# Performance work log

Measured on AMD Instinct MI355X. Metric: run time of the kernel, lower is better.

Reference implementation:

```python
import jax, jax.numpy as jnp
import numpy as np

N_NODES = 100_000
N_EDGES = 1_600_000
F_IN = 32
F_OUT = 32
DIM = 2
K = 5                      # kernel_size per dim (open spline)
KTOT = K ** DIM            # 25 kernel weight matrices
S = 2 ** DIM               # 4 nonzero linear-B-spline basis terms per edge
NEG_SLOPE = 0.2

# offsets over the 2^DIM corners of the spline cell, [S, DIM]
_OFFSETS = np.array([[(s >> d) & 1 for d in range(DIM)] for s in range(S)], dtype=np.int32)
_STRIDES = np.array([K ** d for d in range(DIM)], dtype=np.int32)


def _spline_basis(pseudo):
    """Degree-1 open B-spline basis. pseudo: [E, DIM] in [0,1].
    Returns basis [E, S] and kernel-weight indices widx [E, S]."""
    offsets = jnp.asarray(_OFFSETS)
    strides = jnp.asarray(_STRIDES)
    p = pseudo * (K - 1)                         # open spline scaling
    fl = jnp.floor(p)
    frac = p - fl                                # [E, DIM]
    b = jnp.where(offsets[None] == 0, 1.0 - frac[:, None, :], frac[:, None, :])
    basis = jnp.prod(b, axis=-1)                 # [E, S]
    idx = jnp.clip(fl.astype(jnp.int32)[:, None, :] + offsets[None], 0, K - 1)
    widx = jnp.sum(idx * strides, axis=-1)       # [E, S] in [0, KTOT)
    return basis, widx


def setup_inputs() -> dict:
    key = jax.random.key(0)
    ks = jax.random.split(key, 7)
    x = jax.random.normal(ks[0], (N_NODES, F_IN), dtype=jnp.float32)
    edge_index = jax.random.randint(ks[1], (2, N_EDGES), 0, N_NODES)
    pseudo = jax.random.uniform(ks[2], (N_EDGES, DIM), dtype=jnp.float32)
    bound = 1.0 / np.sqrt(KTOT * F_IN)           # matches reset_parameters uniform(size, ...)
    weight = jax.random.uniform(ks[3], (KTOT, F_IN, F_OUT), jnp.float32, -bound, bound)
    root_weight = jax.random.uniform(ks[4], (F_IN, F_OUT), jnp.float32, -bound, bound)
    att_weight = jax.random.uniform(ks[5], (2 * F_OUT,), jnp.float32, -bound, bound)
    bias = jax.random.uniform(ks[6], (F_OUT,), jnp.float32, -bound, bound)
    return {"x": x, "edge_index": edge_index, "pseudo": pseudo, "weight": weight,
            "root_weight": root_weight, "att_weight": att_weight, "bias": bias}


def reference(x, edge_index, pseudo, weight, root_weight, att_weight, bias):
    row, col = edge_index[0], edge_index[1]      # row = target, col = source
    basis, widx = _spline_basis(pseudo)          # [E,S], [E,S]

    # Precompute x @ W_k for every kernel weight: [N, KTOT, F_OUT]
    xw = jnp.einsum('nf,kfo->nko', x, weight)
    flat = col[:, None] * KTOT + widx            # [E, S] flat (node, kernel) index
    gathered = xw.reshape(-1, F_OUT)[flat]       # [E, S, F_OUT]
    msg = jnp.einsum('es,esf->ef', basis, gathered)  # spline-weighted edge messages

    x_root = x @ root_weight                     # [N, F_OUT]

    # GAT-style attention logits: cat([x_root[row], msg]) . att_weight
    alpha = x_root[row] @ att_weight[:F_OUT] + msg @ att_weight[F_OUT:]
    alpha = jnp.where(alpha > 0, alpha, NEG_SLOPE * alpha)  # leaky relu

    # segment softmax over incoming edges of each target node
    amax = jax.ops.segment_max(alpha, row, num_segments=N_NODES)
    amax = jnp.where(jnp.isfinite(amax), amax, 0.0)
    ex = jnp.exp(alpha - amax[row])
    denom = jax.ops.segment_sum(ex, row, num_segments=N_NODES)
    att = ex / (denom[row] + 1e-16)

    out = jax.ops.segment_sum(msg * att[:, None], row, num_segments=N_NODES)
    return out + x_root + bias
```

## Files before the change

### kernel.cpp

```cpp
#include <hip/hip_runtime.h>
#include <stdint.h>

#define N_NODES 100000
#define N_EDGES 1600000
#define NBLK_SCAN 391

typedef __attribute__((ext_vector_type(8))) short short8;
typedef __attribute__((ext_vector_type(4))) float float4v;

__device__ __forceinline__ unsigned short f32_to_bf16(float f) {
  uint32_t u = __float_as_uint(f);
  u += 0x7fffu + ((u >> 16) & 1u);
  return (unsigned short)(u >> 16);
}
__device__ __forceinline__ float bf16_to_f32(unsigned short h) {
  return __uint_as_float(((uint32_t)h) << 16);
}

__global__ __launch_bounds__(256) void k_zero(
    const float* __restrict__ weight, const float* __restrict__ root_w,
    int* __restrict__ deg, unsigned short* __restrict__ wbf) {
  int tid = threadIdx.x;
  int b = blockIdx.x;
  int i = b * 256 + tid;
  if (i < N_NODES) deg[i] = 0;
  if (b < 100) {
    int e = i;
    int km = e >> 10;
    int rem = e & 1023;
    int kk = rem >> 5;
    int fo = rem & 31;
    int t = km * 2 + (fo >> 4);
    int c = fo & 15;
    int q = kk >> 3, j = kk & 7;
    wbf[((t * 4 + q) * 16 + c) * 8 + j] = f32_to_bf16(weight[e]);
  } else if (b == 100) {
    for (int idx = tid; idx < 1024; idx += 256) {
      int kk = idx >> 5;
      int fo = idx & 31;
      int t = 50 + (fo >> 4);
      int c = fo & 15;
      int q = kk >> 3, j = kk & 7;
      wbf[((t * 4 + q) * 16 + c) * 8 + j] = f32_to_bf16(root_w[idx]);
    }
  }
}

__global__ __launch_bounds__(256) void k1_xw(
    const float* __restrict__ x, const unsigned short* __restrict__ wbf,
    const int* __restrict__ ei, const float* __restrict__ att_w,
    const float* __restrict__ bias,
    int* __restrict__ deg, unsigned short* __restrict__ rank,
    unsigned short* __restrict__ xw, float* __restrict__ out,
    float* __restrict__ r_dot) {
  __shared__ __align__(16) unsigned short ot[16 * 808];
  __shared__ float xr[16][33];
  int tid = threadIdx.x;
  int b = blockIdx.x;

  int e = b * 256 + tid;
  int rk = atomicAdd(&deg[ei[e]], 1);

  int wave = tid >> 6, lane = tid & 63;
  int quad = lane >> 4, c16 = lane & 15;
  int n0 = b * 16;
  const float* xp = x + (size_t)(n0 + c16) * 32 + quad * 8;
  float4 a0 = *reinterpret_cast<const float4*>(xp);
  float4 a1 = *reinterpret_cast<const float4*>(xp + 4);
  short8 af;
  af[0] = (short)f32_to_bf16(a0.x); af[1] = (short)f32_to_bf16(a0.y);
  af[2] = (short)f32_to_bf16(a0.z); af[3] = (short)f32_to_bf16(a0.w);
  af[4] = (short)f32_to_bf16(a1.x); af[5] = (short)f32_to_bf16(a1.y);
  af[6] = (short)f32_to_bf16(a1.z); af[7] = (short)f32_to_bf16(a1.w);

  for (int t = wave; t < 52; t += 4) {
    short8 bf = *reinterpret_cast<const short8*>(wbf + ((t * 4 + quad) * 16 + c16) * 8);
    float4v acc = {0.f, 0.f, 0.f, 0.f};
    acc = __builtin_amdgcn_mfma_f32_16x16x32_bf16(af, bf, acc, 0, 0, 0);
    if (t < 50) {
      int cg = t * 16 + c16;
#pragma unroll
      for (int r = 0; r < 4; r++) ot[(quad * 4 + r) * 808 + cg] = f32_to_bf16(acc[r]);
    } else {
      int f = (t - 50) * 16 + c16;
#pragma unroll
      for (int r = 0; r < 4; r++) xr[quad * 4 + r][f] = acc[r];
    }
  }
  __syncthreads();

  const uint4* src = (const uint4*)ot;
  uint4* dst = (uint4*)(xw + (size_t)n0 * 800);
  for (int i = tid; i < 1600; i += 256) {
    int r = i / 100;
    int c = i - r * 100;
    dst[r * 100 + c] = src[r * 101 + c];
  }
  for (int idx = tid; idx < 512; idx += 256) {
    int n = idx >> 5, f = idx & 31;
    out[(n0 + n) * 32 + f] = xr[n][f] + bias[f];
  }
  if (tid < 16) {
    float s = 0.f;
#pragma unroll
    for (int f = 0; f < 32; f++) s += xr[tid][f] * att_w[f];
    r_dot[n0 + tid] = s;
  }
  rank[e] = (unsigned short)rk;
}

__global__ __launch_bounds__(256) void kscan1(const int* __restrict__ deg,
                                              int* __restrict__ incl,
                                              int* __restrict__ bsum) {
  __shared__ int s[256];
  int tid = threadIdx.x;
  int i = blockIdx.x * 256 + tid;
  int v = (i < N_NODES) ? deg[i] : 0;
  s[tid] = v;
  __syncthreads();
  for (int d = 1; d < 256; d <<= 1) {
    int t = (tid >= d) ? s[tid - d] : 0;
    __syncthreads();
    s[tid] += t;
    __syncthreads();
  }
  if (i < N_NODES) incl[i] = s[tid];
  if (tid == 255) bsum[blockIdx.x] = s[255];
}

__global__ __launch_bounds__(512) void kscan2(const int* __restrict__ bsum,
                                              int* __restrict__ bbase) {
  __shared__ int s[512];
  int tid = threadIdx.x;
  int v = (tid < NBLK_SCAN) ? bsum[tid] : 0;
  s[tid] = v;
  __syncthreads();
  for (int d = 1; d < 512; d <<= 1) {
    int t = (tid >= d) ? s[tid - d] : 0;
    __syncthreads();
    s[tid] += t;
    __syncthreads();
  }
  if (tid < NBLK_SCAN) bbase[tid] = s[tid] - v;
}

__global__ __launch_bounds__(256) void kscan3(const int* __restrict__ deg,
                                              int* __restrict__ offs,
                                              const int* __restrict__ bbase) {
  int i = blockIdx.x * 256 + threadIdx.x;
  if (i < N_NODES) offs[i] = offs[i] - deg[i] + bbase[i >> 8];
  if (i == 0) offs[N_NODES] = N_EDGES;
}

__global__ __launch_bounds__(256) void kscatter(
    const int* __restrict__ ei, const float* __restrict__ pseudo,
    const int* __restrict__ offs, const unsigned short* __restrict__ rank,
    uint2* __restrict__ epack) {
  int tid = threadIdx.x;
  int base = blockIdx.x * 2048;
#pragma unroll
  for (int k = 0; k < 8; k++) {
    int e = base + k * 256 + tid;
    if (e < N_EDGES) {
      int r = ei[e];
      int c = ei[N_EDGES + e];
      int pos = offs[r] + (int)rank[e];
      float p0 = pseudo[2 * e] * 4.f;
      float p1 = pseudo[2 * e + 1] * 4.f;
      float fl0 = floorf(p0), fl1 = floorf(p1);
      float fr0 = p0 - fl0, fr1 = p1 - fl1;
      int i0 = (int)fl0, i1 = (int)fl1;
      int a0 = min(i0, 4), a0p = min(i0 + 1, 4);
      int a1 = 5 * min(i1, 4), a1p = 5 * min(i1 + 1, 4);
      unsigned long long w0 = (unsigned long long)(a0 + a1);
      unsigned long long w1 = (unsigned long long)(a0p + a1);
      unsigned long long w2 = (unsigned long long)(a0 + a1p);
      unsigned long long w3 = (unsigned long long)(a0p + a1p);
      unsigned long long q0 = (unsigned long long)__float2uint_rn(fr0 * 8191.f);
      unsigned long long q1 = (unsigned long long)__float2uint_rn(fr1 * 8191.f);
      unsigned long long v = (unsigned long long)(unsigned int)c |
                             (w0 << 17) | (w1 << 22) | (w2 << 27) | (w3 << 32) |
                             (q0 << 37) | (q1 << 50);
      uint2 pk;
      pk.x = (unsigned int)v;
      pk.y = (unsigned int)(v >> 32);
      epack[pos] = pk;
    }
  }
}

__device__ __forceinline__ void decode_pk(uint2 pk, int& col, int& w0, int& w1,
                                          int& w2, int& w3, float& fr0, float& fr1) {
  unsigned long long v = ((unsigned long long)pk.y << 32) | pk.x;
  col = (int)(v & 0x1FFFF);
  w0 = (int)((v >> 17) & 31); w1 = (int)((v >> 22) & 31);
  w2 = (int)((v >> 27) & 31); w3 = (int)((v >> 32) & 31);
  fr0 = (float)(unsigned int)((v >> 37) & 8191) * (1.f / 8191.f);
  fr1 = (float)(unsigned int)((v >> 50) & 8191) * (1.f / 8191.f);
}

__device__ __forceinline__ void edge_step(uint2 pk, const unsigned short* __restrict__ xwf,
                                          float a2, float rd, float& acc, float& den) {
  int col, w0, w1, w2, w3; float fr0, fr1;
  decode_pk(pk, col, w0, w1, w2, w3, fr0, fr1);
  const unsigned short* base = xwf + (size_t)col * 800;
  float g0 = bf16_to_f32(base[w0 * 32]);
  float g1 = bf16_to_f32(base[w1 * 32]);
  float g2 = bf16_to_f32(base[w2 * 32]);
  float g3 = bf16_to_f32(base[w3 * 32]);
  float c0 = 1.f - fr0, c1 = 1.f - fr1;
  float msg = c1 * (c0 * g0 + fr0 * g1) + fr1 * (c0 * g2 + fr0 * g3);
  float t = msg * a2;
#pragma unroll
  for (int m = 16; m >= 1; m >>= 1) t += __shfl_xor(t, m);
  float alpha = rd + t;
  alpha = alpha > 0.f ? alpha : 0.2f * alpha;
  float ex = __expf(alpha);
  acc += msg * ex;
  den += ex;
}

__global__ __launch_bounds__(256) void k2_csr(
    const int* __restrict__ offs, const uint2* __restrict__ epack,
    const unsigned short* __restrict__ xw, const float* __restrict__ r_dot,
    const float* __restrict__ att_w, float* __restrict__ out) {
  int tid = threadIdx.x;
  int wave = tid >> 6, lane = tid & 63;
  int node = blockIdx.x * 4 + wave;
  if (node >= N_NODES) return;
  int f = lane & 31, half = lane >> 5;
  float a2 = att_w[32 + f];
  float rd = r_dot[node];
  int s0 = offs[node], s1 = offs[node + 1];
  const unsigned short* xwf = xw + f;
  float acc = 0.f, den = 0.f;
  int i = s0 + half;

  for (; i + 6 < s1; i += 8) {
    uint2 p[4];
    p[0] = epack[i];     p[1] = epack[i + 2];
    p[2] = epack[i + 4]; p[3] = epack[i + 6];
    int col[4], w0[4], w1[4], w2[4], w3[4];
    float fr0[4], fr1[4];
#pragma unroll
    for (int u = 0; u < 4; u++)
      decode_pk(p[u], col[u], w0[u], w1[u], w2[u], w3[u], fr0[u], fr1[u]);
    float g0[4], g1[4], g2[4], g3[4];
#pragma unroll
    for (int u = 0; u < 4; u++) {
      const unsigned short* base = xwf + (size_t)col[u] * 800;
      g0[u] = bf16_to_f32(base[w0[u] * 32]);
      g1[u] = bf16_to_f32(base[w1[u] * 32]);
      g2[u] = bf16_to_f32(base[w2[u] * 32]);
      g3[u] = bf16_to_f32(base[w3[u] * 32]);
    }
    float msg[4], t[4];
#pragma unroll
    for (int u = 0; u < 4; u++) {
      float c0 = 1.f - fr0[u], c1 = 1.f - fr1[u];
      msg[u] = c1 * (c0 * g0[u] + fr0[u] * g1[u]) + fr1[u] * (c0 * g2[u] + fr0[u] * g3[u]);
      t[u] = msg[u] * a2;
    }
#pragma unroll
    for (int m = 16; m >= 1; m >>= 1) {
      t[0] += __shfl_xor(t[0], m);
      t[1] += __shfl_xor(t[1], m);
      t[2] += __shfl_xor(t[2], m);
      t[3] += __shfl_xor(t[3], m);
    }
#pragma unroll
    for (int u = 0; u < 4; u++) {
      float alpha = rd + t[u];
      alpha = alpha > 0.f ? alpha : 0.2f * alpha;
      float ex = __expf(alpha);
      acc += msg[u] * ex;
      den += ex;
    }
  }
  for (; i < s1; i += 2) edge_step(epack[i], xwf, a2, rd, acc, den);

  acc += __shfl_xor(acc, 32);
  den += __shfl_xor(den, 32);
  if (half == 0) out[node * 32 + f] += acc / (den + 1e-16f);
}

extern "C" void kernel_launch(void* const* d_in, const int* in_sizes, int n_in,
                              void* d_out, int out_size, void* d_ws, size_t ws_size,
                              hipStream_t stream) {
  const float* x      = (const float*)d_in[0];
  const int*   ei     = (const int*)d_in[1];
  const float* pseudo = (const float*)d_in[2];
  const float* weight = (const float*)d_in[3];
  const float* root_w = (const float*)d_in[4];
  const float* att_w  = (const float*)d_in[5];
  const float* bias   = (const float*)d_in[6];
  float* out = (float*)d_out;

  char* ws = (char*)d_ws;
  unsigned short* xw   = (unsigned short*)ws;
  float* r_dot         = (float*)(ws + 160000000);
  unsigned short* wbf  = (unsigned short*)(ws + 160400000);
  int* deg             = (int*)(ws + 160453504);
  int* offs            = (int*)(ws + 160853504);
  int* bsum            = (int*)(ws + 161253520);
  int* bbase           = (int*)(ws + 161255120);
  unsigned short* rank = (unsigned short*)(ws + 161256720);
  uint2* epack         = (uint2*)(ws + 164456720);

  hipLaunchKernelGGL(k_zero, dim3(NBLK_SCAN), dim3(256), 0, stream,
                     weight, root_w, deg, wbf);
  hipLaunchKernelGGL(k1_xw, dim3(6250), dim3(256), 0, stream,
                     x, wbf, ei, att_w, bias, deg, rank, xw, out, r_dot);
  hipLaunchKernelGGL(kscan1, dim3(NBLK_SCAN), dim3(256), 0, stream, deg, offs, bsum);
  hipLaunchKernelGGL(kscan2, dim3(1), dim3(512), 0, stream, bsum, bbase);
  hipLaunchKernelGGL(kscan3, dim3(NBLK_SCAN), dim3(256), 0, stream, deg, offs, bbase);
  hipLaunchKernelGGL(kscatter, dim3(782), dim3(256), 0, stream,
                     ei, pseudo, offs, rank, epack);
  hipLaunchKernelGGL(k2_csr, dim3(25000), dim3(256), 0, stream,
                     offs, epack, xw, r_dot, att_w, out);
}
```

Before: 336.8 us.

## Precompute per-node attention dots and move softmax exp into scatter; single-pass scan

Projects each node's 25 xw rows onto the attention vector in k1 (ydot). The scatter kernel then computes each edge's attention logit and exp from four bilinear-interpolated scalars and packs the bf16 exp into the edge record. This removes the per-edge 32-lane shuffle reduction and exp from the CSR aggregation kernel. The three-kernel scan is also replaced by a single decoupled-lookback scan, which cuts two launches. The costs are coarser quantisation (8-bit fractions, bf16 exp and ydot), extra ydot storage and gathers, and a spin-wait lookback that relies on tiles being scheduled in order.

```diff
diff --git a/kernel.cpp b/kernel.cpp
--- a/kernel.cpp
+++ b/kernel.cpp
@@ -19,11 +19,14 @@
 
 __global__ __launch_bounds__(256) void k_zero(
     const float* __restrict__ weight, const float* __restrict__ root_w,
-    int* __restrict__ deg, unsigned short* __restrict__ wbf) {
+    int* __restrict__ deg, unsigned short* __restrict__ wbf,
+    unsigned long long* __restrict__ tilepack, int* __restrict__ tilectr) {
   int tid = threadIdx.x;
   int b = blockIdx.x;
   int i = b * 256 + tid;
   if (i < N_NODES) deg[i] = 0;
+  if (i < NBLK_SCAN) tilepack[i] = 0ull;
+  if (i == 0) *tilectr = 0;
   if (b < 100) {
     int e = i;
     int km = e >> 10;
@@ -52,14 +55,17 @@
     const float* __restrict__ bias,
     int* __restrict__ deg, unsigned short* __restrict__ rank,
     unsigned short* __restrict__ xw, float* __restrict__ out,
-    float* __restrict__ r_dot) {
+    float* __restrict__ r_dot, unsigned short* __restrict__ ydot) {
   __shared__ __align__(16) unsigned short ot[16 * 808];
   __shared__ float xr[16][33];
+  __shared__ float a2s[32];
   int tid = threadIdx.x;
   int b = blockIdx.x;
 
   int e = b * 256 + tid;
   int rk = atomicAdd(&deg[ei[e]], 1);
+
+  if (tid < 32) a2s[tid] = att_w[32 + tid];
 
   int wave = tid >> 6, lane = tid & 63;
   int quad = lane >> 4, c16 = lane & 15;
@@ -96,6 +102,14 @@
     int c = i - r * 100;
     dst[r * 100 + c] = src[r * 101 + c];
   }
+  for (int idx = tid; idx < 400; idx += 256) {
+    int n = idx & 15;
+    int k = idx >> 4;
+    float s = 0.f;
+#pragma unroll
+    for (int ff = 0; ff < 32; ff++) s += bf16_to_f32(ot[n * 808 + k * 32 + ff]) * a2s[ff];
+    ydot[(size_t)(n0 + n) * 25 + k] = f32_to_bf16(s);
+  }
   for (int idx = tid; idx < 512; idx += 256) {
     int n = idx >> 5, f = idx & 31;
     out[(n0 + n) * 32 + f] = xr[n][f] + bias[f];
@@ -109,12 +123,16 @@
   rank[e] = (unsigned short)rk;
 }
 
-__global__ __launch_bounds__(256) void kscan1(const int* __restrict__ deg,
-                                              int* __restrict__ incl,
-                                              int* __restrict__ bsum) {
+__global__ __launch_bounds__(256) void k_scan(
+    const int* __restrict__ deg, int* __restrict__ offs,
+    int* __restrict__ tilectr, unsigned long long* __restrict__ tilepack) {
   __shared__ int s[256];
+  __shared__ int sh_tile, sh_excl;
   int tid = threadIdx.x;
-  int i = blockIdx.x * 256 + tid;
+  if (tid == 0) sh_tile = atomicAdd(tilectr, 1);
+  __syncthreads();
+  int tile = sh_tile;
+  int i = tile * 256 + tid;
   int v = (i < N_NODES) ? deg[i] : 0;
   s[tid] = v;
   __syncthreads();
@@ -124,160 +142,127 @@
     s[tid] += t;
     __syncthreads();
   }
-  if (i < N_NODES) incl[i] = s[tid];
-  if (tid == 255) bsum[blockIdx.x] = s[255];
-}
-
-__global__ __launch_bounds__(512) void kscan2(const int* __restrict__ bsum,
-                                              int* __restrict__ bbase) {
-  __shared__ int s[512];
-  int tid = threadIdx.x;
-  int v = (tid < NBLK_SCAN) ? bsum[tid] : 0;
-  s[tid] = v;
+  int incl = s[tid];
+  int agg = s[255];
+  if (tid == 0) {
+    unsigned long long init = ((tile == 0) ? (2ull << 32) : (1ull << 32)) | (unsigned int)agg;
+    __hip_atomic_store(&tilepack[tile], init, __ATOMIC_RELEASE, __HIP_MEMORY_SCOPE_AGENT);
+    if (tile == 0) sh_excl = 0;
+  }
+  if (tile > 0 && tid < 64) {
+    int excl = 0;
+    int base = tile - 1;
+    while (true) {
+      int look = base - tid;
+      unsigned long long pk;
+      if (look >= 0) {
+        do {
+          pk = __hip_atomic_load(&tilepack[look], __ATOMIC_ACQUIRE, __HIP_MEMORY_SCOPE_AGENT);
+        } while ((pk >> 32) == 0);
+      } else {
+        pk = (2ull << 32);
+      }
+      unsigned long long m2 = __ballot((pk >> 32) == 2);
+      int lim = (m2 == 0ull) ? 64 : (__ffsll(m2) - 1);
+      int val = (tid <= lim) ? (int)(unsigned int)pk : 0;
+#pragma unroll
+      for (int m = 1; m < 64; m <<= 1) val += __shfl_xor(val, m);
+      excl += val;
+      if (lim < 64) break;
+      base -= 64;
+    }
+    if (tid == 0) {
+      __hip_atomic_store(&tilepack[tile], (2ull << 32) | (unsigned int)(excl + agg),
+                         __ATOMIC_RELEASE, __HIP_MEMORY_SCOPE_AGENT);
+      sh_excl = excl;
+    }
+  }
   __syncthreads();
-  for (int d = 1; d < 512; d <<= 1) {
-    int t = (tid >= d) ? s[tid - d] : 0;
-    __syncthreads();
-    s[tid] += t;
-    __syncthreads();
-  }
-  if (tid < NBLK_SCAN) bbase[tid] = s[tid] - v;
-}
-
-__global__ __launch_bounds__(256) void kscan3(const int* __restrict__ deg,
-                                              int* __restrict__ offs,
-                                              const int* __restrict__ bbase) {
-  int i = blockIdx.x * 256 + threadIdx.x;
-  if (i < N_NODES) offs[i] = offs[i] - deg[i] + bbase[i >> 8];
-  if (i == 0) offs[N_NODES] = N_EDGES;
+  if (i < N_NODES) offs[i] = sh_excl + incl - v;
+  if (i == N_NODES - 1) offs[N_NODES] = N_EDGES;
 }
 
 __global__ __launch_bounds__(256) void kscatter(
     const int* __restrict__ ei, const float* __restrict__ pseudo,
     const int* __restrict__ offs, const unsigned short* __restrict__ rank,
+    const float* __restrict__ r_dot, const unsigned short* __restrict__ ydot,
     uint2* __restrict__ epack) {
-  int tid = threadIdx.x;
-  int base = blockIdx.x * 2048;
-#pragma unroll
-  for (int k = 0; k < 8; k++) {
-    int e = base + k * 256 + tid;
-    if (e < N_EDGES) {
-      int r = ei[e];
-      int c = ei[N_EDGES + e];
-      int pos = offs[r] + (int)rank[e];
-      float p0 = pseudo[2 * e] * 4.f;
-      float p1 = pseudo[2 * e + 1] * 4.f;
-      float fl0 = floorf(p0), fl1 = floorf(p1);
-      float fr0 = p0 - fl0, fr1 = p1 - fl1;
-      int i0 = (int)fl0, i1 = (int)fl1;
-      int a0 = min(i0, 4), a0p = min(i0 + 1, 4);
-      int a1 = 5 * min(i1, 4), a1p = 5 * min(i1 + 1, 4);
-      unsigned long long w0 = (unsigned long long)(a0 + a1);
-      unsigned long long w1 = (unsigned long long)(a0p + a1);
-      unsigned long long w2 = (unsigned long long)(a0 + a1p);
-      unsigned long long w3 = (unsigned long long)(a0p + a1p);
-      unsigned long long q0 = (unsigned long long)__float2uint_rn(fr0 * 8191.f);
-      unsigned long long q1 = (unsigned long long)__float2uint_rn(fr1 * 8191.f);
-      unsigned long long v = (unsigned long long)(unsigned int)c |
-                             (w0 << 17) | (w1 << 22) | (w2 << 27) | (w3 << 32) |
-                             (q0 << 37) | (q1 << 50);
-      uint2 pk;
-      pk.x = (unsigned int)v;
-      pk.y = (unsigned int)(v >> 32);
-      epack[pos] = pk;
-    }
-  }
-}
-
-__device__ __forceinline__ void decode_pk(uint2 pk, int& col, int& w0, int& w1,
-                                          int& w2, int& w3, float& fr0, float& fr1) {
-  unsigned long long v = ((unsigned long long)pk.y << 32) | pk.x;
-  col = (int)(v & 0x1FFFF);
-  w0 = (int)((v >> 17) & 31); w1 = (int)((v >> 22) & 31);
-  w2 = (int)((v >> 27) & 31); w3 = (int)((v >> 32) & 31);
-  fr0 = (float)(unsigned int)((v >> 37) & 8191) * (1.f / 8191.f);
-  fr1 = (float)(unsigned int)((v >> 50) & 8191) * (1.f / 8191.f);
+  int e = blockIdx.x * 256 + threadIdx.x;
+  int r = ei[e];
+  int c = ei[N_EDGES + e];
+  int pos = offs[r] + (int)rank[e];
+  float p0 = pseudo[2 * e] * 4.f;
+  float p1 = pseudo[2 * e + 1] * 4.f;
+  float fl0 = floorf(p0), fl1 = floorf(p1);
+  float fr0 = p0 - fl0, fr1 = p1 - fl1;
+  int i0 = (int)fl0, i1 = (int)fl1;
+  int j0p = min(i0 + 1, 4);
+  int j1 = 5 * i1, j1p = 5 * min(i1 + 1, 4);
+  int rb = c * 25;
+  float y0 = bf16_to_f32(ydot[rb + i0 + j1]);
+  float y1 = bf16_to_f32(ydot[rb + j0p + j1]);
+  float y2 = bf16_to_f32(ydot[rb + i0 + j1p]);
+  float y3 = bf16_to_f32(ydot[rb + j0p + j1p]);
+  float fm0 = 1.f - fr0, fm1 = 1.f - fr1;
+  float b0 = fm0 * fm1, b1 = fr0 * fm1, b2 = fm0 * fr1, b3 = fr0 * fr1;
+  float alpha = r_dot[r] + b0 * y0 + b1 * y1 + b2 * y2 + b3 * y3;
+  alpha = fmaxf(alpha, 0.2f * alpha);
+  float ex = __expf(alpha);
+  unsigned u = __float_as_uint(ex);
+  unsigned exb = (u + 0x7fffu + ((u >> 16) & 1u)) & 0xffff0000u;
+  unsigned q0 = __float2uint_rn(fr0 * 255.f);
+  unsigned q1 = __float2uint_rn(fr1 * 255.f);
+  uint2 pk;
+  pk.x = (unsigned)c | ((unsigned)i0 << 17) | ((unsigned)i1 << 20) | (q0 << 23);
+  pk.y = exb | q1;
+  epack[pos] = pk;
 }
 
 __device__ __forceinline__ void edge_step(uint2 pk, const unsigned short* __restrict__ xwf,
-                                          float a2, float rd, float& acc, float& den) {
-  int col, w0, w1, w2, w3; float fr0, fr1;
-  decode_pk(pk, col, w0, w1, w2, w3, fr0, fr1);
-  const unsigned short* base = xwf + (size_t)col * 800;
-  float g0 = bf16_to_f32(base[w0 * 32]);
-  float g1 = bf16_to_f32(base[w1 * 32]);
-  float g2 = bf16_to_f32(base[w2 * 32]);
-  float g3 = bf16_to_f32(base[w3 * 32]);
-  float c0 = 1.f - fr0, c1 = 1.f - fr1;
-  float msg = c1 * (c0 * g0 + fr0 * g1) + fr1 * (c0 * g2 + fr0 * g3);
-  float t = msg * a2;
-#pragma unroll
-  for (int m = 16; m >= 1; m >>= 1) t += __shfl_xor(t, m);
-  float alpha = rd + t;
-  alpha = alpha > 0.f ? alpha : 0.2f * alpha;
-  float ex = __expf(alpha);
-  acc += msg * ex;
+                                          float& acc, float& den) {
+  int c  = (int)(pk.x & 0x1FFFF);
+  int i0 = (int)((pk.x >> 17) & 7);
+  int i1 = (int)((pk.x >> 20) & 7);
+  float fr0 = (float)((pk.x >> 23) & 255u) * (1.f / 255.f);
+  float fr1 = (float)(pk.y & 255u) * (1.f / 255.f);
+  float ex = __uint_as_float(pk.y & 0xffff0000u);
+  int j0p = min(i0 + 1, 4);
+  int j1 = 5 * i1, j1p = 5 * min(i1 + 1, 4);
+  int base = c * 800;
+  float g0 = bf16_to_f32(xwf[base + (i0 + j1) * 32]);
+  float g1 = bf16_to_f32(xwf[base + (j0p + j1) * 32]);
+  float g2 = bf16_to_f32(xwf[base + (i0 + j1p) * 32]);
+  float g3 = bf16_to_f32(xwf[base + (j0p + j1p) * 32]);
+  float fm0 = 1.f - fr0, fm1 = 1.f - fr1;
+  float msg = fm1 * (fm0 * g0 + fr0 * g1) + fr1 * (fm0 * g2 + fr0 * g3);
+  acc = fmaf(msg, ex, acc);
   den += ex;
 }
 
 __global__ __launch_bounds__(256) void k2_csr(
     const int* __restrict__ offs, const uint2* __restrict__ epack,
-    const unsigned short* __restrict__ xw, const float* __restrict__ r_dot,
-    const float* __restrict__ att_w, float* __restrict__ out) {
+    const unsigned short* __restrict__ xw, float* __restrict__ out) {
   int tid = threadIdx.x;
   int wave = tid >> 6, lane = tid & 63;
   int node = blockIdx.x * 4 + wave;
   if (node >= N_NODES) return;
   int f = lane & 31, half = lane >> 5;
-  float a2 = att_w[32 + f];
-  float rd = r_dot[node];
   int s0 = offs[node], s1 = offs[node + 1];
   const unsigned short* xwf = xw + f;
   float acc = 0.f, den = 0.f;
   int i = s0 + half;
 
   for (; i + 6 < s1; i += 8) {
-    uint2 p[4];
-    p[0] = epack[i];     p[1] = epack[i + 2];
-    p[2] = epack[i + 4]; p[3] = epack[i + 6];
-    int col[4], w0[4], w1[4], w2[4], w3[4];
-    float fr0[4], fr1[4];
-#pragma unroll
-    for (int u = 0; u < 4; u++)
-      decode_pk(p[u], col[u], w0[u], w1[u], w2[u], w3[u], fr0[u], fr1[u]);
-    float g0[4], g1[4], g2[4], g3[4];
-#pragma unroll
-    for (int u = 0; u < 4; u++) {
-      const unsigned short* base = xwf + (size_t)col[u] * 800;
-      g0[u] = bf16_to_f32(base[w0[u] * 32]);
-      g1[u] = bf16_to_f32(base[w1[u] * 32]);
-      g2[u] = bf16_to_f32(base[w2[u] * 32]);
-      g3[u] = bf16_to_f32(base[w3[u] * 32]);
-    }
-    float msg[4], t[4];
-#pragma unroll
-    for (int u = 0; u < 4; u++) {
-      float c0 = 1.f - fr0[u], c1 = 1.f - fr1[u];
-      msg[u] = c1 * (c0 * g0[u] + fr0[u] * g1[u]) + fr1[u] * (c0 * g2[u] + fr0[u] * g3[u]);
-      t[u] = msg[u] * a2;
-    }
-#pragma unroll
-    for (int m = 16; m >= 1; m >>= 1) {
-      t[0] += __shfl_xor(t[0], m);
-      t[1] += __shfl_xor(t[1], m);
-      t[2] += __shfl_xor(t[2], m);
-      t[3] += __shfl_xor(t[3], m);
-    }
-#pragma unroll
-    for (int u = 0; u < 4; u++) {
-      float alpha = rd + t[u];
-      alpha = alpha > 0.f ? alpha : 0.2f * alpha;
-      float ex = __expf(alpha);
-      acc += msg[u] * ex;
-      den += ex;
-    }
-  }
-  for (; i < s1; i += 2) edge_step(epack[i], xwf, a2, rd, acc, den);
+    uint2 p0 = epack[i];
+    uint2 p1 = epack[i + 2];
+    uint2 p2 = epack[i + 4];
+    uint2 p3 = epack[i + 6];
+    edge_step(p0, xwf, acc, den);
+    edge_step(p1, xwf, acc, den);
+    edge_step(p2, xwf, acc, den);
+    edge_step(p3, xwf, acc, den);
+  }
+  for (; i < s1; i += 2) edge_step(epack[i], xwf, acc, den);
 
   acc += __shfl_xor(acc, 32);
   den += __shfl_xor(den, 32);
@@ -300,22 +285,22 @@
   unsigned short* xw   = (unsigned short*)ws;
   float* r_dot         = (float*)(ws + 160000000);
   unsigned short* wbf  = (unsigned short*)(ws + 160400000);
-  int* deg             = (int*)(ws + 160453504);
-  int* offs            = (int*)(ws + 160853504);
-  int* bsum            = (int*)(ws + 161253520);
-  int* bbase           = (int*)(ws + 161255120);
-  unsigned short* rank = (unsigned short*)(ws + 161256720);
-  uint2* epack         = (uint2*)(ws + 164456720);
+  int* deg             = (int*)(ws + 160453248);
+  int* offs            = (int*)(ws + 160853248);
+  unsigned long long* tilepack = (unsigned long long*)(ws + 161253264);
+  int* tilectr         = (int*)(ws + 161256392);
+  unsigned short* rank = (unsigned short*)(ws + 161256400);
+  unsigned short* ydot = (unsigned short*)(ws + 164456400);
+  uint2* epack         = (uint2*)(ws + 169456400);
 
   hipLaunchKernelGGL(k_zero, dim3(NBLK_SCAN), dim3(256), 0, stream,
-                     weight, root_w, deg, wbf);
+                     weight, root_w, deg, wbf, tilepack, tilectr);
   hipLaunchKernelGGL(k1_xw, dim3(6250), dim3(256), 0, stream,
-                     x, wbf, ei, att_w, bias, deg, rank, xw, out, r_dot);
-  hipLaunchKernelGGL(kscan1, dim3(NBLK_SCAN), dim3(256), 0, stream, deg, offs, bsum);
-  hipLaunchKernelGGL(kscan2, dim3(1), dim3(512), 0, stream, bsum, bbase);
-  hipLaunchKernelGGL(kscan3, dim3(NBLK_SCAN), dim3(256), 0, stream, deg, offs, bbase);
-  hipLaunchKernelGGL(kscatter, dim3(782), dim3(256), 0, stream,
-                     ei, pseudo, offs, rank, epack);
+                     x, wbf, ei, att_w, bias, deg, rank, xw, out, r_dot, ydot);
+  hipLaunchKernelGGL(k_scan, dim3(NBLK_SCAN), dim3(256), 0, stream,
+                     deg, offs, tilectr, tilepack);
+  hipLaunchKernelGGL(kscatter, dim3(6250), dim3(256), 0, stream,
+                     ei, pseudo, offs, rank, r_dot, ydot, epack);
   hipLaunchKernelGGL(k2_csr, dim3(25000), dim3(256), 0, stream,
-                     offs, epack, xw, r_dot, att_w, out);
-}
+                     offs, epack, xw, out);
+}
```

Result: slower. 356.7 us (+5.9%).
